# Kernel tuning notes

Measured on AMD Instinct MI355X. Metric: run time of the kernel, lower is better.

## Reference

```python
import jax, jax.numpy as jnp
import numpy as np
import math

D_MODEL = 2048
HEADS = 16
D_K = D_MODEL // HEADS  # 128
D_FF = 2048
N = 8192
EPS = 1e-6


def _norm(x, alpha, bias):
    # torch Norm: alpha * (x - mean) / (std + eps) + bias, std uses ddof=1
    mu = jnp.mean(x, axis=-1, keepdims=True)
    sd = jnp.std(x, axis=-1, ddof=1, keepdims=True)
    return alpha * (x - mu) / (sd + EPS) + bias


def setup_inputs() -> dict:
    key = jax.random.key(0)
    ks = jax.random.split(key, 16)
    s = 0.02
    inp = {
        "q": jax.random.normal(ks[0], (N, D_MODEL), jnp.float32),
        "k": jax.random.normal(ks[1], (N, D_MODEL), jnp.float32),
        "v": jax.random.normal(ks[2], (N, D_MODEL), jnp.float32),
        # norm params (norm_1 exists in module but is unused in forward)
        "nq_a": jnp.ones((D_MODEL,), jnp.float32), "nq_b": jnp.zeros((D_MODEL,), jnp.float32),
        "nk_a": jnp.ones((D_MODEL,), jnp.float32), "nk_b": jnp.zeros((D_MODEL,), jnp.float32),
        "nv_a": jnp.ones((D_MODEL,), jnp.float32), "nv_b": jnp.zeros((D_MODEL,), jnp.float32),
        "n2_a": jnp.ones((D_MODEL,), jnp.float32), "n2_b": jnp.zeros((D_MODEL,), jnp.float32),
        # attention projections, stored [in, out]
        "Wq": jax.random.normal(ks[3], (D_MODEL, D_MODEL), jnp.float32) * s,
        "bq": jnp.zeros((D_MODEL,), jnp.float32),
        "Wk": jax.random.normal(ks[4], (D_MODEL, D_MODEL), jnp.float32) * s,
        "bk": jnp.zeros((D_MODEL,), jnp.float32),
        "Wv": jax.random.normal(ks[5], (D_MODEL, D_MODEL), jnp.float32) * s,
        "bv": jnp.zeros((D_MODEL,), jnp.float32),
        "Wo": jax.random.normal(ks[6], (D_MODEL, D_MODEL), jnp.float32) * s,
        "bo": jnp.zeros((D_MODEL,), jnp.float32),
        # FFN
        "W1": jax.random.normal(ks[7], (D_MODEL, D_FF), jnp.float32) * s,
        "b1": jnp.zeros((D_FF,), jnp.float32),
        "W2": jax.random.normal(ks[8], (D_FF, D_MODEL), jnp.float32) * s,
        "b2": jnp.zeros((D_MODEL,), jnp.float32),
    }
    return inp


def reference(q, k, v,
              nq_a, nq_b, nk_a, nk_b, nv_a, nv_b, n2_a, n2_b,
              Wq, bq, Wk, bk, Wv, bv, Wo, bo, W1, b1, W2, b2):
    x = v  # residual stream (dropout is identity at inference)
    qn = _norm(q, nq_a, nq_b)
    kn = _norm(k, nk_a, nk_b)
    vn = _norm(v, nv_a, nv_b)

    # projections -> [N, h, d_k] then transpose(1,2) -> [N, d_k, h]
    qh = (qn @ Wq + bq).reshape(N, HEADS, D_K).transpose(0, 2, 1)
    kh = (kn @ Wk + bk).reshape(N, HEADS, D_K).transpose(0, 2, 1)
    vh = (vn @ Wv + bv).reshape(N, HEADS, D_K).transpose(0, 2, 1)

    # NON-STANDARD (as-written in source): per-token [d_k, d_k] attention
    # contracting over the head axis, scaled by 1/sqrt(d_k).
    scores = jnp.einsum('nah,nbh->nab', qh, kh) / math.sqrt(D_K)  # [N, d_k, d_k]
    probs = jax.nn.softmax(scores, axis=-1)
    attn = jnp.einsum('nab,nbh->nah', probs, vh)  # [N, d_k, h]

    concat = attn.transpose(0, 2, 1).reshape(N, D_MODEL)  # [N, h*d_k]
    x = x + (concat @ Wo + bo)

    x2 = _norm(x, n2_a, n2_b)
    ff = jax.nn.relu(x2 @ W1 + b1) @ W2 + b2
    return x + ff
```

## Files before the change

kernel.cpp:

```cpp
#include <hip/hip_runtime.h>
#include <hip/hip_bf16.h>

#define DM 2048
#define NTOK 8192
#define EPS 1e-6f

typedef __attribute__((ext_vector_type(8))) short short8;
typedef __attribute__((ext_vector_type(4))) short short4v;
typedef __attribute__((ext_vector_type(4))) float f32x4;
typedef __attribute__((ext_vector_type(16))) float f32x16;
typedef __attribute__((ext_vector_type(4))) unsigned int u32x4;

typedef const __attribute__((address_space(1))) void gvoid;
typedef __attribute__((address_space(3))) void lvoid;

static __device__ __forceinline__ unsigned short f2bf(float f) {
    unsigned u = __builtin_bit_cast(unsigned, f);
    unsigned r = u + 0x7FFFu + ((u >> 16) & 1u);
    return (unsigned short)(r >> 16);
}
static __device__ __forceinline__ float bf2f(unsigned short h) {
    return __builtin_bit_cast(float, (unsigned)h << 16);
}

__global__ __launch_bounds__(256) void norm_rows(
        const float* __restrict__ in, const float* __restrict__ alpha,
        const float* __restrict__ beta, unsigned short* __restrict__ out) {
    const int row = blockIdx.x;
    const int t = threadIdx.x;
    const float* x = in + (size_t)row * DM + t * 8;
    float4 v0 = *(const float4*)(x);
    float4 v1 = *(const float4*)(x + 4);
    float s = (v0.x + v0.y) + (v0.z + v0.w) + (v1.x + v1.y) + (v1.z + v1.w);
    float ss = v0.x*v0.x + v0.y*v0.y + v0.z*v0.z + v0.w*v0.w
             + v1.x*v1.x + v1.y*v1.y + v1.z*v1.z + v1.w*v1.w;
    #pragma unroll
    for (int m = 1; m < 64; m <<= 1) {
        s  += __shfl_xor(s, m);
        ss += __shfl_xor(ss, m);
    }
    __shared__ float red[8];
    const int wv = t >> 6, ln = t & 63;
    if (ln == 0) { red[wv] = s; red[4 + wv] = ss; }
    __syncthreads();
    s  = (red[0] + red[1]) + (red[2] + red[3]);
    ss = (red[4] + red[5]) + (red[6] + red[7]);
    const float mu = s * (1.0f / DM);
    float var = (ss - s * mu) * (1.0f / (DM - 1));
    var = fmaxf(var, 0.0f);
    const float scale = 1.0f / (sqrtf(var) + EPS);
    float4 a0 = *(const float4*)(alpha + t*8);
    float4 a1 = *(const float4*)(alpha + t*8 + 4);
    float4 b0 = *(const float4*)(beta + t*8);
    float4 b1 = *(const float4*)(beta + t*8 + 4);
    short8 o;
    o[0] = (short)f2bf(a0.x * (v0.x - mu) * scale + b0.x);
    o[1] = (short)f2bf(a0.y * (v0.y - mu) * scale + b0.y);
    o[2] = (short)f2bf(a0.z * (v0.z - mu) * scale + b0.z);
    o[3] = (short)f2bf(a0.w * (v0.w - mu) * scale + b0.w);
    o[4] = (short)f2bf(a1.x * (v1.x - mu) * scale + b1.x);
    o[5] = (short)f2bf(a1.y * (v1.y - mu) * scale + b1.y);
    o[6] = (short)f2bf(a1.z * (v1.z - mu) * scale + b1.z);
    o[7] = (short)f2bf(a1.w * (v1.w - mu) * scale + b1.w);
    *(short8*)(out + (size_t)row * DM + t * 8) = o;
}

__global__ __launch_bounds__(256) void norm_rows_bf16(
        const unsigned short* __restrict__ in, const float* __restrict__ alpha,
        const float* __restrict__ beta, unsigned short* __restrict__ out) {
    const int row = blockIdx.x;
    const int t = threadIdx.x;
    short8 rv = *(const short8*)(in + (size_t)row * DM + t * 8);
    float xv[8];
    #pragma unroll
    for (int j = 0; j < 8; ++j) xv[j] = bf2f((unsigned short)rv[j]);
    float s = 0.f, ss = 0.f;
    #pragma unroll
    for (int j = 0; j < 8; ++j) { s += xv[j]; ss += xv[j]*xv[j]; }
    #pragma unroll
    for (int m = 1; m < 64; m <<= 1) {
        s  += __shfl_xor(s, m);
        ss += __shfl_xor(ss, m);
    }
    __shared__ float red[8];
    const int wv = t >> 6, ln = t & 63;
    if (ln == 0) { red[wv] = s; red[4 + wv] = ss; }
    __syncthreads();
    s  = (red[0] + red[1]) + (red[2] + red[3]);
    ss = (red[4] + red[5]) + (red[6] + red[7]);
    const float mu = s * (1.0f / DM);
    float var = (ss - s * mu) * (1.0f / (DM - 1));
    var = fmaxf(var, 0.0f);
    const float scale = 1.0f / (sqrtf(var) + EPS);
    short8 o;
    #pragma unroll
    for (int j = 0; j < 8; ++j) {
        const float av = alpha[t*8 + j], bv = beta[t*8 + j];
        o[j] = (short)f2bf(av * (xv[j] - mu) * scale + bv);
    }
    *(short8*)(out + (size_t)row * DM + t * 8) = o;
}

__global__ __launch_bounds__(256) void wtrans6(
        const float* __restrict__ Wq, const float* __restrict__ Wk,
        const float* __restrict__ Wv, const float* __restrict__ Wo,
        const float* __restrict__ W1, const float* __restrict__ W2,
        unsigned short* __restrict__ Tq, unsigned short* __restrict__ Tk,
        unsigned short* __restrict__ Tv, unsigned short* __restrict__ To,
        unsigned short* __restrict__ T1, unsigned short* __restrict__ T2,
        float isq) {
    __shared__ float tile[32][33];
    const int z = blockIdx.z;
    const float* W = z==0?Wq: z==1?Wk: z==2?Wv: z==3?Wo: z==4?W1: W2;
    unsigned short* Wt = z==0?Tq: z==1?Tk: z==2?Tv: z==3?To: z==4?T1: T2;
    const int perm = (z < 2) ? 1 : 0;
    const float ws = (z == 0) ? isq : 1.0f;
    const int bc = blockIdx.x * 32, bk = blockIdx.y * 32;
    const int t = threadIdx.x;
    const int tc = t & 31, tr = t >> 5;
    #pragma unroll
    for (int i = 0; i < 4; ++i)
        tile[tr + i*8][tc] = W[(size_t)(bk + tr + i*8) * DM + bc + tc];
    __syncthreads();
    #pragma unroll
    for (int i = 0; i < 4; ++i) {
        const int c = bc + tr + i*8;
        const int pc = perm ? ((c & 127) * 16 + (c >> 7)) : c;
        Wt[(size_t)pc * DM + bk + tc] = f2bf(tile[tc][tr + i*8] * ws);
    }
}

#define BARRIER __builtin_amdgcn_s_barrier()
#define VMCNT(n) asm volatile("s_waitcnt vmcnt(" #n ")" ::: "memory")

template<int EPI>
__global__ __launch_bounds__(512, 2) void gemm256(
        const unsigned short* __restrict__ A, const unsigned short* __restrict__ Bt,
        const float* __restrict__ bias, const float* __restrict__ residF,
        const unsigned short* __restrict__ residB,
        float* __restrict__ outF, unsigned short* __restrict__ outB, int biasPerm,
        float bscale) {
    __shared__ __align__(16) char lds[131072];
    char* ldsA = lds;
    char* ldsB = lds + 65536;

    const int t = threadIdx.x, l = t & 63, w = t >> 6;
    const int wm = w >> 2, wn = w & 3;

    const int b = blockIdx.x;
    const int xcd = b & 7;
    const int j = b >> 3;
    const int m0 = (xcd * 4 + (j & 3)) * 256;
    const int n0 = (j >> 2) * 256;

    const int rS = t >> 3;
    const int cS = ((t & 7) ^ (rS & 7)) * 8;
    const unsigned short* aSt = A  + (size_t)(m0 + rS) * 2048 + cS;
    const unsigned short* bSt = Bt + (size_t)(n0 + rS) * 2048 + cS;
    const int ldsStW = w * 1024;

    const int aRd = wm * 16384 + (l & 15) * 128;
    const int bRd = (wn >> 1) * 16384 + (wn & 1) * 8192 + (l & 15) * 128;
    const int ch0 = (((l >> 4) + 0) ^ (l & 7)) * 16;
    const int ch1 = (((l >> 4) + 4) ^ (l & 7)) * 16;

    short8 af[8][2], bf[4][2];
    f32x4 acc[8][4] = {};

#define STG_A(buf, h, kt) do { \
    __builtin_amdgcn_global_load_lds((gvoid*)(aSt + (size_t)((h)*128)*2048 + (kt)*64), \
        (lvoid*)(ldsA + (buf)*32768 + (h)*16384 + ldsStW), 16, 0, 0); \
    __builtin_amdgcn_global_load_lds((gvoid*)(aSt + (size_t)((h)*128+64)*2048 + (kt)*64), \
        (lvoid*)(ldsA + (buf)*32768 + (h)*16384 + 8192 + ldsStW), 16, 0, 0); \
} while(0)
#define STG_B(buf, h, kt) do { \
    __builtin_amdgcn_global_load_lds((gvoid*)(bSt + (size_t)((h)*128)*2048 + (kt)*64), \
        (lvoid*)(ldsB + (buf)*32768 + (h)*16384 + ldsStW), 16, 0, 0); \
    __builtin_amdgcn_global_load_lds((gvoid*)(bSt + (size_t)((h)*128+64)*2048 + (kt)*64), \
        (lvoid*)(ldsB + (buf)*32768 + (h)*16384 + 8192 + ldsStW), 16, 0, 0); \
} while(0)
#define RD_A(buf, mh) do { \
    _Pragma("unroll") for (int ml = 0; ml < 4; ++ml) { \
        af[(mh)*4+ml][0] = *(const short8*)(ldsA + (buf)*32768 + aRd + ((mh)*4+ml)*2048 + ch0); \
        af[(mh)*4+ml][1] = *(const short8*)(ldsA + (buf)*32768 + aRd + ((mh)*4+ml)*2048 + ch1); \
    } } while(0)
#define RD_B(buf, nh) do { \
    _Pragma("unroll") for (int nl = 0; nl < 2; ++nl) { \
        bf[(nh)*2+nl][0] = *(const short8*)(ldsB + (buf)*32768 + bRd + ((nh)*2+nl)*2048 + ch0); \
        bf[(nh)*2+nl][1] = *(const short8*)(ldsB + (buf)*32768 + bRd + ((nh)*2+nl)*2048 + ch1); \
    } } while(0)
#define MM_Q(mh, nh) do { \
    _Pragma("unroll") for (int ml = 0; ml < 4; ++ml) \
    _Pragma("unroll") for (int nl = 0; nl < 2; ++nl) { \
        acc[(mh)*4+ml][(nh)*2+nl] = __builtin_amdgcn_mfma_f32_16x16x32_bf16( \
            af[(mh)*4+ml][0], bf[(nh)*2+nl][0], acc[(mh)*4+ml][(nh)*2+nl], 0, 0, 0); \
        acc[(mh)*4+ml][(nh)*2+nl] = __builtin_amdgcn_mfma_f32_16x16x32_bf16( \
            af[(mh)*4+ml][1], bf[(nh)*2+nl][1], acc[(mh)*4+ml][(nh)*2+nl], 0, 0, 0); \
    } \
} while(0)

#define KSTEP(c, kt) do { \
    RD_A(c, 0); RD_B(c, 0); \
    __builtin_amdgcn_s_setprio(1); \
    MM_Q(0, 0); \
    RD_B(c, 1); \
    MM_Q(0, 1); \
    RD_A(c, 1); \
    MM_Q(1, 1); \
    MM_Q(1, 0); \
    __builtin_amdgcn_s_setprio(0); \
    BARRIER; \
    if ((kt) + 2 < 32) { \
        STG_A(c, 0, (kt)+2); STG_A(c, 1, (kt)+2); \
        STG_B(c, 0, (kt)+2); STG_B(c, 1, (kt)+2); \
        VMCNT(8); \
    } else { \
        VMCNT(0); \
    } \
    BARRIER; \
} while(0)

    STG_A(0, 0, 0); STG_A(0, 1, 0); STG_B(0, 0, 0); STG_B(0, 1, 0);
    STG_A(1, 0, 1); STG_A(1, 1, 1); STG_B(1, 0, 1); STG_B(1, 1, 1);
    VMCNT(8);
    BARRIER;

    #pragma unroll 1
    for (int i = 0; i < 16; ++i) {
        KSTEP(0, 2*i);
        KSTEP(1, 2*i + 1);
    }

    unsigned short* cs = (unsigned short*)lds;
    #pragma unroll 1
    for (int pass = 0; pass < 2; ++pass) {
        BARRIER;
        if (wm == pass) {
            #pragma unroll
            for (int ni = 0; ni < 4; ++ni) {
                const int col = wn*64 + ni*16 + (l & 15);
                const int gcol = n0 + col;
                const int cb = biasPerm ? ((gcol >> 4) + (gcol & 15) * 128) : gcol;
                const float bvv = bias[cb] * bscale;
                #pragma unroll
                for (int mi = 0; mi < 8; ++mi) {
                    #pragma unroll
                    for (int r = 0; r < 4; ++r) {
                        const int row = mi*16 + (l >> 4)*4 + r;
                        float vv = acc[mi][ni][r] + bvv;
                        if (EPI == 1) vv = fmaxf(vv, 0.0f);
                        cs[row*260 + col] = f2bf(vv);
                    }
                }
            }
        }
        BARRIER;
        #pragma unroll
        for (int s = 0; s < 8; ++s) {
            const int row = (t >> 5) + s*16;
            const int seg = t & 31;
            short8 pk = *(const short8*)(cs + row*260 + seg*8);
            const int grow = m0 + pass*128 + row;
            const size_t gb = (size_t)grow * 2048 + n0 + seg*8;
            if (EPI == 3) {
                float4 r0 = *(const float4*)(residF + gb);
                float4 r1 = *(const float4*)(residF + gb + 4);
                short8 o;
                o[0] = (short)f2bf(bf2f((unsigned short)pk[0]) + r0.x);
                o[1] = (short)f2bf(bf2f((unsigned short)pk[1]) + r0.y);
                o[2] = (short)f2bf(bf2f((unsigned short)pk[2]) + r0.z);
                o[3] = (short)f2bf(bf2f((unsigned short)pk[3]) + r0.w);
                o[4] = (short)f2bf(bf2f((unsigned short)pk[4]) + r1.x);
                o[5] = (short)f2bf(bf2f((unsigned short)pk[5]) + r1.y);
                o[6] = (short)f2bf(bf2f((unsigned short)pk[6]) + r1.z);
                o[7] = (short)f2bf(bf2f((unsigned short)pk[7]) + r1.w);
                *(short8*)(outB + gb) = o;
            } else if (EPI == 4) {
                short8 rb = *(const short8*)(residB + gb);
                float4 o0, o1;
                o0.x = bf2f((unsigned short)pk[0]) + bf2f((unsigned short)rb[0]);
                o0.y = bf2f((unsigned short)pk[1]) + bf2f((unsigned short)rb[1]);
                o0.z = bf2f((unsigned short)pk[2]) + bf2f((unsigned short)rb[2]);
                o0.w = bf2f((unsigned short)pk[3]) + bf2f((unsigned short)rb[3]);
                o1.x = bf2f((unsigned short)pk[4]) + bf2f((unsigned short)rb[4]);
                o1.y = bf2f((unsigned short)pk[5]) + bf2f((unsigned short)rb[5]);
                o1.z = bf2f((unsigned short)pk[6]) + bf2f((unsigned short)rb[6]);
                o1.w = bf2f((unsigned short)pk[7]) + bf2f((unsigned short)rb[7]);
                *(float4*)(outF + gb) = o0;
                *(float4*)(outF + gb + 4) = o1;
            } else {
                *(short8*)(outB + gb) = pk;
            }
        }
    }
#undef KSTEP
#undef STG_A
#undef STG_B
#undef RD_A
#undef RD_B
#undef MM_Q
}

__global__ __launch_bounds__(256) void attn_tok(
        const unsigned short* __restrict__ Qt, const unsigned short* __restrict__ Kt,
        const unsigned short* __restrict__ Vp, unsigned short* __restrict__ Cc) {
    const int n = blockIdx.x;
    const int t = threadIdx.x, w = t >> 6, l = t & 63;
    const int q31 = l & 31, hi = l >> 5;
    __shared__ __align__(16) unsigned short c_s[16 * 132];

    const size_t tb = (size_t)n * DM;
    const short8 qf = *(const short8*)(Qt + tb + (w*32 + q31)*16 + hi*8);
    short8 kf[4];
    #pragma unroll
    for (int bt = 0; bt < 4; ++bt)
        kf[bt] = *(const short8*)(Kt + tb + (bt*32 + q31)*16 + hi*8);
    short8 vf[8];
    #pragma unroll
    for (int ks = 0; ks < 8; ++ks)
        vf[ks] = *(const short8*)(Vp + tb + (q31 & 15)*128 + ks*16 + hi*8);

    const f32x16 z = {};
    f32x16 sc[4];
    #pragma unroll
    for (int bt = 0; bt < 4; ++bt)
        sc[bt] = __builtin_amdgcn_mfma_f32_32x32x16_bf16(kf[bt], qf, z, 0, 0, 0);

    float m0 = sc[0][0], m1 = sc[1][0], m2 = sc[2][0], m3 = sc[3][0];
    #pragma unroll
    for (int r = 1; r < 16; ++r) {
        m0 = fmaxf(m0, sc[0][r]); m1 = fmaxf(m1, sc[1][r]);
        m2 = fmaxf(m2, sc[2][r]); m3 = fmaxf(m3, sc[3][r]);
    }
    float mx = fmaxf(fmaxf(m0, m1), fmaxf(m2, m3));
    { float a2 = mx, b2 = mx;
      asm volatile("v_permlane32_swap_b32 %0, %1" : "+v"(a2), "+v"(b2));
      mx = fmaxf(a2, b2); }

    float p[4][16];
    float s0 = 0.f, s1 = 0.f, s2 = 0.f, s3 = 0.f;
    #pragma unroll
    for (int r = 0; r < 16; ++r) {
        p[0][r] = __expf(sc[0][r] - mx); s0 += p[0][r];
        p[1][r] = __expf(sc[1][r] - mx); s1 += p[1][r];
        p[2][r] = __expf(sc[2][r] - mx); s2 += p[2][r];
        p[3][r] = __expf(sc[3][r] - mx); s3 += p[3][r];
    }
    float sm = (s0 + s1) + (s2 + s3);
    { float a2 = sm, b2 = sm;
      asm volatile("v_permlane32_swap_b32 %0, %1" : "+v"(a2), "+v"(b2));
      sm = a2 + b2; }
    const float inv = __builtin_amdgcn_rcpf(sm);
    #pragma unroll
    for (int bt = 0; bt < 4; ++bt)
        #pragma unroll
        for (int r = 0; r < 16; ++r)
            p[bt][r] *= inv;

    f32x16 acc = {};
    #pragma unroll
    for (int ks = 0; ks < 8; ++ks) {
        const int bt = ks >> 1, r0 = (ks & 1) * 8;
        unsigned X0, Y0, X1, Y1;
        asm("v_cvt_pk_bf16_f32 %0, %1, %2" : "=v"(X0) : "v"(p[bt][r0+0]), "v"(p[bt][r0+1]));
        asm("v_cvt_pk_bf16_f32 %0, %1, %2" : "=v"(Y0) : "v"(p[bt][r0+4]), "v"(p[bt][r0+5]));
        asm("v_cvt_pk_bf16_f32 %0, %1, %2" : "=v"(X1) : "v"(p[bt][r0+2]), "v"(p[bt][r0+3]));
        asm("v_cvt_pk_bf16_f32 %0, %1, %2" : "=v"(Y1) : "v"(p[bt][r0+6]), "v"(p[bt][r0+7]));
        asm volatile("v_permlane32_swap_b32 %0, %1" : "+v"(X0), "+v"(Y0));
        asm volatile("v_permlane32_swap_b32 %0, %1" : "+v"(X1), "+v"(Y1));
        u32x4 pw; pw[0] = X0; pw[1] = X1; pw[2] = Y0; pw[3] = Y1;
        const short8 paf = __builtin_bit_cast(short8, pw);
        acc = __builtin_amdgcn_mfma_f32_32x32x16_bf16(paf, vf[ks], acc, 0, 0, 0);
    }

    if (q31 < 16) {
        #pragma unroll
        for (int rp = 0; rp < 8; ++rp) {
            const int r = rp * 2;
            const int a = (r & 3) + 8 * (r >> 2) + 4 * hi;
            unsigned pk;
            asm("v_cvt_pk_bf16_f32 %0, %1, %2" : "=v"(pk) : "v"(acc[r]), "v"(acc[r+1]));
            *(unsigned*)((char*)c_s + q31*264 + (w*32 + a)*2) = pk;
        }
    }
    __syncthreads();
    *(short8*)(Cc + tb + t*8) = *(const short8*)((char*)c_s + (t >> 4)*264 + (t & 15)*16);
}

extern "C" void kernel_launch(void* const* d_in, const int* in_sizes, int n_in,
                              void* d_out, int out_size, void* d_ws, size_t ws_size,
                              hipStream_t stream) {
    (void)in_sizes; (void)n_in; (void)out_size; (void)ws_size;
    const float* q    = (const float*)d_in[0];
    const float* k    = (const float*)d_in[1];
    const float* v    = (const float*)d_in[2];
    const float* nq_a = (const float*)d_in[3];
    const float* nq_b = (const float*)d_in[4];
    const float* nk_a = (const float*)d_in[5];
    const float* nk_b = (const float*)d_in[6];
    const float* nv_a = (const float*)d_in[7];
    const float* nv_b = (const float*)d_in[8];
    const float* n2_a = (const float*)d_in[9];
    const float* n2_b = (const float*)d_in[10];
    const float* Wq   = (const float*)d_in[11];
    const float* bq   = (const float*)d_in[12];
    const float* Wk   = (const float*)d_in[13];
    const float* bk   = (const float*)d_in[14];
    const float* Wv   = (const float*)d_in[15];
    const float* bv   = (const float*)d_in[16];
    const float* Wo   = (const float*)d_in[17];
    const float* bo   = (const float*)d_in[18];
    const float* W1   = (const float*)d_in[19];
    const float* b1   = (const float*)d_in[20];
    const float* W2   = (const float*)d_in[21];
    const float* b2   = (const float*)d_in[22];

    char* ws = (char*)d_ws;
    const size_t MB = 1024 * 1024;
    unsigned short* buf0 = (unsigned short*)(ws);
    unsigned short* QtB  = (unsigned short*)(ws + 32*MB);
    unsigned short* KtB  = (unsigned short*)(ws + 64*MB);
    unsigned short* VpB  = (unsigned short*)(ws + 96*MB);
    unsigned short* Wqt  = (unsigned short*)(ws + 128*MB);
    unsigned short* Wkt  = (unsigned short*)(ws + 136*MB);
    unsigned short* Wvt  = (unsigned short*)(ws + 144*MB);
    unsigned short* Wot  = (unsigned short*)(ws + 152*MB);
    unsigned short* W1t  = (unsigned short*)(ws + 160*MB);
    unsigned short* W2t  = (unsigned short*)(ws + 168*MB);
    unsigned short* x2   = QtB;
    unsigned short* h1   = KtB;
    unsigned short* xb   = VpB;
    float* x = (float*)d_out;

    const float isq = 0.088388347648318447f;

    dim3 b256(256);
    dim3 gT6(DM / 32, DM / 32, 6);
    wtrans6<<<gT6, b256, 0, stream>>>(Wq, Wk, Wv, Wo, W1, W2,
                                      Wqt, Wkt, Wvt, Wot, W1t, W2t, isq);

    dim3 gN(NTOK);
    dim3 gG(256);
    dim3 b512(512);

    norm_rows<<<gN, b256, 0, stream>>>(q, nq_a, nq_b, buf0);
    gemm256<0><<<gG, b512, 0, stream>>>(buf0, Wqt, bq, nullptr, nullptr, nullptr, QtB, 1, isq);
    norm_rows<<<gN, b256, 0, stream>>>(k, nk_a, nk_b, buf0);
    gemm256<0><<<gG, b512, 0, stream>>>(buf0, Wkt, bk, nullptr, nullptr, nullptr, KtB, 1, 1.0f);
    norm_rows<<<gN, b256, 0, stream>>>(v, nv_a, nv_b, buf0);
    gemm256<0><<<gG, b512, 0, stream>>>(buf0, Wvt, bv, nullptr, nullptr, nullptr, VpB, 0, 1.0f);
    attn_tok<<<gN, b256, 0, stream>>>(QtB, KtB, VpB, buf0);
    gemm256<3><<<gG, b512, 0, stream>>>(buf0, Wot, bo, v, nullptr, nullptr, xb, 0, 1.0f);
    norm_rows_bf16<<<gN, b256, 0, stream>>>(xb, n2_a, n2_b, x2);
    gemm256<1><<<gG, b512, 0, stream>>>(x2, W1t, b1, nullptr, nullptr, nullptr, h1, 0, 1.0f);
    gemm256<4><<<gG, b512, 0, stream>>>(h1, W2t, b2, nullptr, xb, x, nullptr, 0, 1.0f);
}
```

Before: 566.6 us.

## Replace 256x256 GEMM with 128x128 tile kernel and simpler double buffering

Swaps the 512-thread 256x256-tile GEMM for a 256-thread 128x128-tile kernel launched with 1024 blocks. It uses a simpler double-buffer scheme that prefetches the next k-tile before computing the current one, with one barrier per step, and writes the epilogue in a single pass. The aim is better occupancy and load balance with less LDS per block. The cost is lower arithmetic intensity per tile and more global/L2 traffic.

```diff
diff --git a/kernel.cpp b/kernel.cpp
--- a/kernel.cpp
+++ b/kernel.cpp
@@ -130,28 +130,25 @@
     }
 }
 
-#define BARRIER __builtin_amdgcn_s_barrier()
-#define VMCNT(n) asm volatile("s_waitcnt vmcnt(" #n ")" ::: "memory")
-
 template<int EPI>
-__global__ __launch_bounds__(512, 2) void gemm256(
+__global__ __launch_bounds__(256, 2) void gemm128(
         const unsigned short* __restrict__ A, const unsigned short* __restrict__ Bt,
         const float* __restrict__ bias, const float* __restrict__ residF,
         const unsigned short* __restrict__ residB,
         float* __restrict__ outF, unsigned short* __restrict__ outB, int biasPerm,
         float bscale) {
-    __shared__ __align__(16) char lds[131072];
+    __shared__ __align__(16) char lds[65536];
     char* ldsA = lds;
-    char* ldsB = lds + 65536;
+    char* ldsB = lds + 32768;
 
     const int t = threadIdx.x, l = t & 63, w = t >> 6;
-    const int wm = w >> 2, wn = w & 3;
+    const int wm = w >> 1, wn = w & 1;
 
     const int b = blockIdx.x;
     const int xcd = b & 7;
     const int j = b >> 3;
-    const int m0 = (xcd * 4 + (j & 3)) * 256;
-    const int n0 = (j >> 2) * 256;
+    const int m0 = (xcd * 8 + (j & 7)) * 128;
+    const int n0 = (j >> 3) * 128;
 
     const int rS = t >> 3;
     const int cS = ((t & 7) ^ (rS & 7)) * 8;
@@ -159,71 +156,44 @@
     const unsigned short* bSt = Bt + (size_t)(n0 + rS) * 2048 + cS;
     const int ldsStW = w * 1024;
 
-    const int aRd = wm * 16384 + (l & 15) * 128;
-    const int bRd = (wn >> 1) * 16384 + (wn & 1) * 8192 + (l & 15) * 128;
+    const int aRd = wm * 8192 + (l & 15) * 128;
+    const int bRd = wn * 8192 + (l & 15) * 128;
     const int ch0 = (((l >> 4) + 0) ^ (l & 7)) * 16;
     const int ch1 = (((l >> 4) + 4) ^ (l & 7)) * 16;
 
-    short8 af[8][2], bf[4][2];
-    f32x4 acc[8][4] = {};
-
-#define STG_A(buf, h, kt) do { \
-    __builtin_amdgcn_global_load_lds((gvoid*)(aSt + (size_t)((h)*128)*2048 + (kt)*64), \
-        (lvoid*)(ldsA + (buf)*32768 + (h)*16384 + ldsStW), 16, 0, 0); \
-    __builtin_amdgcn_global_load_lds((gvoid*)(aSt + (size_t)((h)*128+64)*2048 + (kt)*64), \
-        (lvoid*)(ldsA + (buf)*32768 + (h)*16384 + 8192 + ldsStW), 16, 0, 0); \
+    short8 af[4][2], bf[4][2];
+    f32x4 acc[4][4] = {};
+
+#define STG(c, kt) do { \
+    _Pragma("unroll") for (int ii = 0; ii < 4; ++ii) { \
+        __builtin_amdgcn_global_load_lds((gvoid*)(aSt + (size_t)(ii*32)*2048 + (size_t)(kt)*64), \
+            (lvoid*)(ldsA + (c)*16384 + ii*4096 + ldsStW), 16, 0, 0); \
+        __builtin_amdgcn_global_load_lds((gvoid*)(bSt + (size_t)(ii*32)*2048 + (size_t)(kt)*64), \
+            (lvoid*)(ldsB + (c)*16384 + ii*4096 + ldsStW), 16, 0, 0); \
+    } } while(0)
+
+#define KSTEP(c, kt) do { \
+    if ((kt) + 1 < 32) STG((c)^1, (kt)+1); \
+    _Pragma("unroll") for (int ml = 0; ml < 4; ++ml) { \
+        af[ml][0] = *(const short8*)(ldsA + (c)*16384 + aRd + ml*2048 + ch0); \
+        af[ml][1] = *(const short8*)(ldsA + (c)*16384 + aRd + ml*2048 + ch1); \
+        bf[ml][0] = *(const short8*)(ldsB + (c)*16384 + bRd + ml*2048 + ch0); \
+        bf[ml][1] = *(const short8*)(ldsB + (c)*16384 + bRd + ml*2048 + ch1); \
+    } \
+    __builtin_amdgcn_s_setprio(1); \
+    _Pragma("unroll") for (int ml = 0; ml < 4; ++ml) \
+    _Pragma("unroll") for (int nl = 0; nl < 4; ++nl) { \
+        acc[ml][nl] = __builtin_amdgcn_mfma_f32_16x16x32_bf16( \
+            af[ml][0], bf[nl][0], acc[ml][nl], 0, 0, 0); \
+        acc[ml][nl] = __builtin_amdgcn_mfma_f32_16x16x32_bf16( \
+            af[ml][1], bf[nl][1], acc[ml][nl], 0, 0, 0); \
+    } \
+    __builtin_amdgcn_s_setprio(0); \
+    __syncthreads(); \
 } while(0)
-#define STG_B(buf, h, kt) do { \
-    __builtin_amdgcn_global_load_lds((gvoid*)(bSt + (size_t)((h)*128)*2048 + (kt)*64), \
-        (lvoid*)(ldsB + (buf)*32768 + (h)*16384 + ldsStW), 16, 0, 0); \
-    __builtin_amdgcn_global_load_lds((gvoid*)(bSt + (size_t)((h)*128+64)*2048 + (kt)*64), \
-        (lvoid*)(ldsB + (buf)*32768 + (h)*16384 + 8192 + ldsStW), 16, 0, 0); \
-} while(0)
-#define RD_A(buf, mh) do { \
-    _Pragma("unroll") for (int ml = 0; ml < 4; ++ml) { \
-        af[(mh)*4+ml][0] = *(const short8*)(ldsA + (buf)*32768 + aRd + ((mh)*4+ml)*2048 + ch0); \
-        af[(mh)*4+ml][1] = *(const short8*)(ldsA + (buf)*32768 + aRd + ((mh)*4+ml)*2048 + ch1); \
-    } } while(0)
-#define RD_B(buf, nh) do { \
-    _Pragma("unroll") for (int nl = 0; nl < 2; ++nl) { \
-        bf[(nh)*2+nl][0] = *(const short8*)(ldsB + (buf)*32768 + bRd + ((nh)*2+nl)*2048 + ch0); \
-        bf[(nh)*2+nl][1] = *(const short8*)(ldsB + (buf)*32768 + bRd + ((nh)*2+nl)*2048 + ch1); \
-    } } while(0)
-#define MM_Q(mh, nh) do { \
-    _Pragma("unroll") for (int ml = 0; ml < 4; ++ml) \
-    _Pragma("unroll") for (int nl = 0; nl < 2; ++nl) { \
-        acc[(mh)*4+ml][(nh)*2+nl] = __builtin_amdgcn_mfma_f32_16x16x32_bf16( \
-            af[(mh)*4+ml][0], bf[(nh)*2+nl][0], acc[(mh)*4+ml][(nh)*2+nl], 0, 0, 0); \
-        acc[(mh)*4+ml][(nh)*2+nl] = __builtin_amdgcn_mfma_f32_16x16x32_bf16( \
-            af[(mh)*4+ml][1], bf[(nh)*2+nl][1], acc[(mh)*4+ml][(nh)*2+nl], 0, 0, 0); \
-    } \
-} while(0)
-
-#define KSTEP(c, kt) do { \
-    RD_A(c, 0); RD_B(c, 0); \
-    __builtin_amdgcn_s_setprio(1); \
-    MM_Q(0, 0); \
-    RD_B(c, 1); \
-    MM_Q(0, 1); \
-    RD_A(c, 1); \
-    MM_Q(1, 1); \
-    MM_Q(1, 0); \
-    __builtin_amdgcn_s_setprio(0); \
-    BARRIER; \
-    if ((kt) + 2 < 32) { \
-        STG_A(c, 0, (kt)+2); STG_A(c, 1, (kt)+2); \
-        STG_B(c, 0, (kt)+2); STG_B(c, 1, (kt)+2); \
-        VMCNT(8); \
-    } else { \
-        VMCNT(0); \
-    } \
-    BARRIER; \
-} while(0)
-
-    STG_A(0, 0, 0); STG_A(0, 1, 0); STG_B(0, 0, 0); STG_B(0, 1, 0);
-    STG_A(1, 0, 1); STG_A(1, 1, 1); STG_B(1, 0, 1); STG_B(1, 1, 1);
-    VMCNT(8);
-    BARRIER;
+
+    STG(0, 0);
+    __syncthreads();
 
     #pragma unroll 1
     for (int i = 0; i < 16; ++i) {
@@ -232,73 +202,63 @@
     }
 
     unsigned short* cs = (unsigned short*)lds;
-    #pragma unroll 1
-    for (int pass = 0; pass < 2; ++pass) {
-        BARRIER;
-        if (wm == pass) {
+    #pragma unroll
+    for (int ni = 0; ni < 4; ++ni) {
+        const int col = wn*64 + ni*16 + (l & 15);
+        const int gcol = n0 + col;
+        const int cb = biasPerm ? ((gcol >> 4) + (gcol & 15) * 128) : gcol;
+        const float bvv = bias[cb] * bscale;
+        #pragma unroll
+        for (int mi = 0; mi < 4; ++mi) {
             #pragma unroll
-            for (int ni = 0; ni < 4; ++ni) {
-                const int col = wn*64 + ni*16 + (l & 15);
-                const int gcol = n0 + col;
-                const int cb = biasPerm ? ((gcol >> 4) + (gcol & 15) * 128) : gcol;
-                const float bvv = bias[cb] * bscale;
-                #pragma unroll
-                for (int mi = 0; mi < 8; ++mi) {
-                    #pragma unroll
-                    for (int r = 0; r < 4; ++r) {
-                        const int row = mi*16 + (l >> 4)*4 + r;
-                        float vv = acc[mi][ni][r] + bvv;
-                        if (EPI == 1) vv = fmaxf(vv, 0.0f);
-                        cs[row*260 + col] = f2bf(vv);
-                    }
-                }
+            for (int r = 0; r < 4; ++r) {
+                const int row = wm*64 + mi*16 + (l >> 4)*4 + r;
+                float vv = acc[mi][ni][r] + bvv;
+                if (EPI == 1) vv = fmaxf(vv, 0.0f);
+                cs[row*132 + col] = f2bf(vv);
             }
         }
-        BARRIER;
-        #pragma unroll
-        for (int s = 0; s < 8; ++s) {
-            const int row = (t >> 5) + s*16;
-            const int seg = t & 31;
-            short8 pk = *(const short8*)(cs + row*260 + seg*8);
-            const int grow = m0 + pass*128 + row;
-            const size_t gb = (size_t)grow * 2048 + n0 + seg*8;
-            if (EPI == 3) {
-                float4 r0 = *(const float4*)(residF + gb);
-                float4 r1 = *(const float4*)(residF + gb + 4);
-                short8 o;
-                o[0] = (short)f2bf(bf2f((unsigned short)pk[0]) + r0.x);
-                o[1] = (short)f2bf(bf2f((unsigned short)pk[1]) + r0.y);
-                o[2] = (short)f2bf(bf2f((unsigned short)pk[2]) + r0.z);
-                o[3] = (short)f2bf(bf2f((unsigned short)pk[3]) + r0.w);
-                o[4] = (short)f2bf(bf2f((unsigned short)pk[4]) + r1.x);
-                o[5] = (short)f2bf(bf2f((unsigned short)pk[5]) + r1.y);
-                o[6] = (short)f2bf(bf2f((unsigned short)pk[6]) + r1.z);
-                o[7] = (short)f2bf(bf2f((unsigned short)pk[7]) + r1.w);
-                *(short8*)(outB + gb) = o;
-            } else if (EPI == 4) {
-                short8 rb = *(const short8*)(residB + gb);
-                float4 o0, o1;
-                o0.x = bf2f((unsigned short)pk[0]) + bf2f((unsigned short)rb[0]);
-                o0.y = bf2f((unsigned short)pk[1]) + bf2f((unsigned short)rb[1]);
-                o0.z = bf2f((unsigned short)pk[2]) + bf2f((unsigned short)rb[2]);
-                o0.w = bf2f((unsigned short)pk[3]) + bf2f((unsigned short)rb[3]);
-                o1.x = bf2f((unsigned short)pk[4]) + bf2f((unsigned short)rb[4]);
-                o1.y = bf2f((unsigned short)pk[5]) + bf2f((unsigned short)rb[5]);
-                o1.z = bf2f((unsigned short)pk[6]) + bf2f((unsigned short)rb[6]);
-                o1.w = bf2f((unsigned short)pk[7]) + bf2f((unsigned short)rb[7]);
-                *(float4*)(outF + gb) = o0;
-                *(float4*)(outF + gb + 4) = o1;
-            } else {
-                *(short8*)(outB + gb) = pk;
-            }
+    }
+    __syncthreads();
+    #pragma unroll
+    for (int s = 0; s < 8; ++s) {
+        const int row = (t >> 4) + s*16;
+        const int seg = t & 15;
+        short8 pk = *(const short8*)(cs + row*132 + seg*8);
+        const int grow = m0 + row;
+        const size_t gb = (size_t)grow * 2048 + n0 + seg*8;
+        if (EPI == 3) {
+            float4 r0 = *(const float4*)(residF + gb);
+            float4 r1 = *(const float4*)(residF + gb + 4);
+            short8 o;
+            o[0] = (short)f2bf(bf2f((unsigned short)pk[0]) + r0.x);
+            o[1] = (short)f2bf(bf2f((unsigned short)pk[1]) + r0.y);
+            o[2] = (short)f2bf(bf2f((unsigned short)pk[2]) + r0.z);
+            o[3] = (short)f2bf(bf2f((unsigned short)pk[3]) + r0.w);
+            o[4] = (short)f2bf(bf2f((unsigned short)pk[4]) + r1.x);
+            o[5] = (short)f2bf(bf2f((unsigned short)pk[5]) + r1.y);
+            o[6] = (short)f2bf(bf2f((unsigned short)pk[6]) + r1.z);
+            o[7] = (short)f2bf(bf2f((unsigned short)pk[7]) + r1.w);
+            *(short8*)(outB + gb) = o;
+        } else if (EPI == 4) {
+            short8 rb = *(const short8*)(residB + gb);
+            float4 o0, o1;
+            o0.x = bf2f((unsigned short)pk[0]) + bf2f((unsigned short)rb[0]);
+            o0.y = bf2f((unsigned short)pk[1]) + bf2f((unsigned short)rb[1]);
+            o0.z = bf2f((unsigned short)pk[2]) + bf2f((unsigned short)rb[2]);
+            o0.w = bf2f((unsigned short)pk[3]) + bf2f((unsigned short)rb[3]);
+            o1.x = bf2f((unsigned short)pk[4]) + bf2f((unsigned short)rb[4]);
+            o1.y = bf2f((unsigned short)pk[5]) + bf2f((unsigned short)rb[5]);
+            o1.z = bf2f((unsigned short)pk[6]) + bf2f((unsigned short)rb[6]);
+            o1.w = bf2f((unsigned short)pk[7]) + bf2f((unsigned short)rb[7]);
+            *(float4*)(outF + gb) = o0;
+            *(float4*)(outF + gb + 4) = o1;
+        } else {
+            *(short8*)(outB + gb) = pk;
         }
     }
+#undef STG
 #undef KSTEP
-#undef STG_A
-#undef STG_B
-#undef RD_A
-#undef RD_B
-#undef MM_Q
 }
 
 __global__ __launch_bounds__(256) void attn_tok(
@@ -440,18 +400,17 @@
                                       Wqt, Wkt, Wvt, Wot, W1t, W2t, isq);
 
     dim3 gN(NTOK);
-    dim3 gG(256);
-    dim3 b512(512);
+    dim3 gG(1024);
 
     norm_rows<<<gN, b256, 0, stream>>>(q, nq_a, nq_b, buf0);
-    gemm256<0><<<gG, b512, 0, stream>>>(buf0, Wqt, bq, nullptr, nullptr, nullptr, QtB, 1, isq);
+    gemm128<0><<<gG, b256, 0, stream>>>(buf0, Wqt, bq, nullptr, nullptr, nullptr, QtB, 1, isq);
     norm_rows<<<gN, b256, 0, stream>>>(k, nk_a, nk_b, buf0);
-    gemm256<0><<<gG, b512, 0, stream>>>(buf0, Wkt, bk, nullptr, nullptr, nullptr, KtB, 1, 1.0f);
+    gemm128<0><<<gG, b256, 0, stream>>>(buf0, Wkt, bk, nullptr, nullptr, nullptr, KtB, 1, 1.0f);
     norm_rows<<<gN, b256, 0, stream>>>(v, nv_a, nv_b, buf0);
-    gemm256<0><<<gG, b512, 0, stream>>>(buf0, Wvt, bv, nullptr, nullptr, nullptr, VpB, 0, 1.0f);
+    gemm128<0><<<gG, b256, 0, stream>>>(buf0, Wvt, bv, nullptr, nullptr, nullptr, VpB, 0, 1.0f);
     attn_tok<<<gN, b256, 0, stream>>>(QtB, KtB, VpB, buf0);
-    gemm256<3><<<gG, b512, 0, stream>>>(buf0, Wot, bo, v, nullptr, nullptr, xb, 0, 1.0f);
+    gemm128<3><<<gG, b256, 0, stream>>>(buf0, Wot, bo, v, nullptr, nullptr, xb, 0, 1.0f);
     norm_rows_bf16<<<gN, b256, 0, stream>>>(xb, n2_a, n2_b, x2);
-    gemm256<1><<<gG, b512, 0, stream>>>(x2, W1t, b1, nullptr, nullptr, nullptr, h1, 0, 1.0f);
-    gemm256<4><<<gG, b512, 0, stream>>>(h1, W2t, b2, nullptr, xb, x, nullptr, 0, 1.0f);
-}
+    gemm128<1><<<gG, b256, 0, stream>>>(x2, W1t, b1, nullptr, nullptr, nullptr, h1, 0, 1.0f);
+    gemm128<4><<<gG, b256, 0, stream>>>(h1, W2t, b2, nullptr, xb, x, nullptr, 0, 1.0f);
+}
```

Result: slower. 652.2 us (+15.1%).
